# Kernel optimization log

Hardware: AMD Instinct MI355X
Metric: run time of the kernel (lower is better)

The kernel has to match this reference:

```python
import jax, jax.numpy as jnp
import numpy as np

B, D, NQ, NK, K = 8, 384, 2048, 2048, 8
NEG_SLOPE = 0.2


def setup_inputs() -> dict:
    key = jax.random.key(0)
    ks = jax.random.split(key, 6)
    return {
        "query_coords": jax.random.normal(ks[0], (B, 3, NQ), jnp.float32),
        "query_features": jax.random.normal(ks[1], (B, D, NQ), jnp.float32),
        "key_coords": jax.random.normal(ks[2], (B, 3, NK), jnp.float32),
        "key_features": jax.random.normal(ks[3], (B, D, NK), jnp.float32),
        "W": jax.random.normal(ks[4], (D, 2 * D), jnp.float32) / np.sqrt(2.0 * D),
        "b": jnp.zeros((D,), jnp.float32),
    }


def _knn_idx(qc, kc, k):
    # qc: [B,3,Nq], kc: [B,3,Nk] -> indices of k nearest keys per query [B,Nq,k]
    q2 = jnp.sum(qc * qc, axis=1)                      # [B,Nq]
    k2 = jnp.sum(kc * kc, axis=1)                      # [B,Nk]
    inner = jnp.einsum('bcq,bck->bqk', qc, kc)         # [B,Nq,Nk]
    dist = q2[:, :, None] - 2.0 * inner + k2[:, None, :]
    _, idx = jax.lax.top_k(-dist, k)
    return idx


def reference(query_coords, query_features, key_coords, key_features, W, b):
    idx = _knn_idx(query_coords, key_coords, K)        # [B,Nq,K]
    kf = jnp.transpose(key_features, (0, 2, 1))        # [B,Nk,D]
    qf = jnp.transpose(query_features, (0, 2, 1))      # [B,Nq,D]
    nbr = jax.vmap(lambda f, i: f[i])(kf, idx)         # gather -> [B,Nq,K,D]
    center = qf[:, :, None, :]                          # [B,Nq,1,D]
    # DGCNN/PoinTr graph feature: concat(neighbor - center, center)
    geom = jnp.concatenate(
        [nbr - center, jnp.broadcast_to(center, nbr.shape)], axis=-1)  # [B,Nq,K,2D]
    h = jnp.einsum('bqkf,df->bqkd', geom, W) + b        # Linear(2D -> D)
    h = jnp.where(h >= 0, h, NEG_SLOPE * h)             # LeakyReLU(0.2)
    return jnp.max(h, axis=2)                           # max over k -> [B,Nq,D]
```

## Files before the change

kernel.cpp:

```cpp
#include <hip/hip_runtime.h>
#include <hip/hip_bf16.h>
#include <float.h>

#define BB 8
#define DD 384
#define NQ 2048
#define NK 2048
#define NEG 0.2f

#define QPW 4

__global__ __launch_bounds__(256) void knn_kernel(
    const float* __restrict__ qc,
    const float* __restrict__ kc,
    int* __restrict__ idx)
{
  __shared__ float4 ksm[NK];

  const int b = blockIdx.y;
  const int t = threadIdx.x;

  const float* kcb = kc + (size_t)b * 3 * NK;
  for (int i = t; i < NK; i += 256) {
    float x = kcb[i], y = kcb[NK + i], z = kcb[2 * NK + i];
    ksm[i] = make_float4(x, y, z, (x * x + y * y) + z * z);
  }
  __syncthreads();

  const int w = t >> 6;
  const int l = t & 63;
  const float* qcb = qc + (size_t)b * 3 * NQ;

  for (int qi = 0; qi < QPW; ++qi) {
    const int q = blockIdx.x * (4 * QPW) + w * QPW + qi;
    const float qx = qcb[q], qy = qcb[NQ + q], qz = qcb[2 * NQ + q];
    const float q2 = (qx * qx + qy * qy) + qz * qz;

    float d[32];
    #pragma unroll
    for (int j = 0; j < 32; ++j) {
      float4 kv = ksm[j * 64 + l];
      float inner = (qx * kv.x + qy * kv.y) + qz * kv.z;
      d[j] = (q2 - 2.0f * inner) + kv.w;
    }

    int outk[8];
    #pragma unroll
    for (int r = 0; r < 8; ++r) {
      float m = d[0]; int mj = 0;
      #pragma unroll
      for (int j = 1; j < 32; ++j) {
        bool c = d[j] < m;
        m  = c ? d[j] : m;
        mj = c ? j : mj;
      }
      int mkey = mj * 64 + l;
      #pragma unroll
      for (int off = 32; off >= 1; off >>= 1) {
        float om = __shfl_xor(m, off);
        int   ok = __shfl_xor(mkey, off);
        bool take = (om < m) || (om == m && ok < mkey);
        m    = take ? om : m;
        mkey = take ? ok : mkey;
      }
      outk[r] = mkey;
      const bool mine = (l == (mkey & 63));
      const int  slot = mkey >> 6;
      #pragma unroll
      for (int j = 0; j < 32; ++j) {
        bool kill = mine && (j == slot);
        d[j] = kill ? FLT_MAX : d[j];
      }
    }

    int myv = outk[0];
    #pragma unroll
    for (int r = 1; r < 8; ++r) myv = (l == r) ? outk[r] : myv;
    if (l < 8) idx[((size_t)b * NQ + q) * 8 + l] = myv;
  }
}

__global__ __launch_bounds__(256) void proj_gemm_all(
    const float* __restrict__ kf,
    const float* __restrict__ qf,
    const float* __restrict__ W,
    const float* __restrict__ bias,
    float* __restrict__ pk,
    float* __restrict__ pq)
{
  __shared__ float At[16][128];
  __shared__ float Bt[16][132];

  const int t    = threadIdx.x;
  const int z    = blockIdx.z;
  const int b    = z & 7;
  const int mode = z >> 3;
  const int n0 = blockIdx.x * 128;
  const int d0 = blockIdx.y * 128;
  const int td = t & 15;
  const int tn = t >> 4;

  float acc[8][8];
  #pragma unroll
  for (int i = 0; i < 8; ++i)
    #pragma unroll
    for (int j = 0; j < 8; ++j) acc[i][j] = 0.f;

  const float* feats = mode ? qf : kf;
  float* out = mode ? pq : pk;
  const float* fb = feats + (size_t)b * DD * 2048;

  const int ar  = t >> 5;
  const int ac  = (t & 31) * 4;
  const int bdl = t >> 2;
  const int bf  = (t & 3) * 4;

  float4 sa0, sa1, sw1a, sw1b, sw2a, sw2b;

#define PREFETCH(KT)                                                           \
  {                                                                            \
    sa0 = *(const float4*)&fb[(size_t)((KT) + ar) * 2048 + n0 + ac];           \
    sa1 = *(const float4*)&fb[(size_t)((KT) + ar + 8) * 2048 + n0 + ac];       \
    const float* wr0 = W + (size_t)(d0 + bdl) * (2 * DD) + (KT) + bf;          \
    const float* wr1 = W + (size_t)(d0 + bdl + 64) * (2 * DD) + (KT) + bf;     \
    sw1a = *(const float4*)wr0;                                                \
    sw1b = *(const float4*)wr1;                                                \
    if (mode) { sw2a = *(const float4*)(wr0 + DD); sw2b = *(const float4*)(wr1 + DD); } \
  }

  PREFETCH(0);

  for (int kt = 0; kt < DD; kt += 16) {
    *(float4*)&At[ar][ac]     = sa0;
    *(float4*)&At[ar + 8][ac] = sa1;
    {
      float4 w = sw1a;
      if (mode) { w.x = sw2a.x - w.x; w.y = sw2a.y - w.y; w.z = sw2a.z - w.z; w.w = sw2a.w - w.w; }
      Bt[bf + 0][bdl] = w.x; Bt[bf + 1][bdl] = w.y;
      Bt[bf + 2][bdl] = w.z; Bt[bf + 3][bdl] = w.w;
    }
    {
      float4 w = sw1b;
      if (mode) { w.x = sw2b.x - w.x; w.y = sw2b.y - w.y; w.z = sw2b.z - w.z; w.w = sw2b.w - w.w; }
      Bt[bf + 0][bdl + 64] = w.x; Bt[bf + 1][bdl + 64] = w.y;
      Bt[bf + 2][bdl + 64] = w.z; Bt[bf + 3][bdl + 64] = w.w;
    }
    __syncthreads();

    if (kt + 16 < DD) PREFETCH(kt + 16);

    #pragma unroll
    for (int k = 0; k < 16; ++k) {
      float a[8], bb[8];
      {
        float4 v = *(const float4*)&At[k][tn * 4];
        a[0] = v.x; a[1] = v.y; a[2] = v.z; a[3] = v.w;
        v = *(const float4*)&At[k][tn * 4 + 64];
        a[4] = v.x; a[5] = v.y; a[6] = v.z; a[7] = v.w;
        v = *(const float4*)&Bt[k][td * 4];
        bb[0] = v.x; bb[1] = v.y; bb[2] = v.z; bb[3] = v.w;
        v = *(const float4*)&Bt[k][td * 4 + 64];
        bb[4] = v.x; bb[5] = v.y; bb[6] = v.z; bb[7] = v.w;
      }
      #pragma unroll
      for (int i = 0; i < 8; ++i)
        #pragma unroll
        for (int j = 0; j < 8; ++j)
          acc[i][j] = fmaf(a[i], bb[j], acc[i][j]);
    }
    __syncthreads();
  }
#undef PREFETCH

  float4 blo = make_float4(0.f, 0.f, 0.f, 0.f);
  float4 bhi = make_float4(0.f, 0.f, 0.f, 0.f);
  if (mode) {
    blo = *(const float4*)&bias[d0 + td * 4];
    bhi = *(const float4*)&bias[d0 + td * 4 + 64];
  }

  float* ob = out + (size_t)b * 2048 * DD;
  #pragma unroll
  for (int i = 0; i < 8; ++i) {
    int n = n0 + tn * 4 + (i & 3) + ((i >= 4) ? 64 : 0);
    float4 c0, c1;
    c0.x = acc[i][0] + blo.x; c0.y = acc[i][1] + blo.y;
    c0.z = acc[i][2] + blo.z; c0.w = acc[i][3] + blo.w;
    c1.x = acc[i][4] + bhi.x; c1.y = acc[i][5] + bhi.y;
    c1.z = acc[i][6] + bhi.z; c1.w = acc[i][7] + bhi.w;
    *(float4*)&ob[(size_t)n * DD + d0 + td * 4]      = c0;
    *(float4*)&ob[(size_t)n * DD + d0 + td * 4 + 64] = c1;
  }
}

__global__ __launch_bounds__(384) void gather_max_kernel(
    const float4* __restrict__ pk4,
    const float4* __restrict__ pq4,
    const int* __restrict__ idx,
    float4* __restrict__ out4)
{
  const int t   = threadIdx.x;
  const int bq0 = blockIdx.x * 4;
  __shared__ int nb[4][8];
  if (t < 32) nb[t >> 3][t & 7] = idx[(size_t)(bq0 + (t >> 3)) * 8 + (t & 7)];
  __syncthreads();

  const int q_l = t / 96;
  const int dv  = t - q_l * 96;
  const int bq  = bq0 + q_l;
  const int b   = bq >> 11;
  const float4* pkb = pk4 + (size_t)b * NK * 96;

  float4 m = make_float4(-FLT_MAX, -FLT_MAX, -FLT_MAX, -FLT_MAX);
  #pragma unroll
  for (int s = 0; s < 8; ++s) {
    float4 v = pkb[(size_t)nb[q_l][s] * 96 + dv];
    m.x = fmaxf(m.x, v.x); m.y = fmaxf(m.y, v.y);
    m.z = fmaxf(m.z, v.z); m.w = fmaxf(m.w, v.w);
  }
  float4 c = pq4[(size_t)bq * 96 + dv];
  float4 r;
  r.x = m.x + c.x; r.y = m.y + c.y; r.z = m.z + c.z; r.w = m.w + c.w;
  r.x = (r.x >= 0.f) ? r.x : NEG * r.x;
  r.y = (r.y >= 0.f) ? r.y : NEG * r.y;
  r.z = (r.z >= 0.f) ? r.z : NEG * r.z;
  r.w = (r.w >= 0.f) ? r.w : NEG * r.w;
  out4[(size_t)bq * 96 + dv] = r;
}

extern "C" void kernel_launch(void* const* d_in, const int* in_sizes, int n_in,
                              void* d_out, int out_size, void* d_ws, size_t ws_size,
                              hipStream_t stream) {
  const float* qc   = (const float*)d_in[0];
  const float* qf   = (const float*)d_in[1];
  const float* kc   = (const float*)d_in[2];
  const float* kf   = (const float*)d_in[3];
  const float* W    = (const float*)d_in[4];
  const float* bias = (const float*)d_in[5];
  float* out = (float*)d_out;

  char* ws = (char*)d_ws;
  float* pk = (float*)ws;
  float* pq = (float*)(ws + (size_t)BB * NK * DD * 4);
  int*   ix = (int*)  (ws + (size_t)2 * BB * NK * DD * 4);

  knn_kernel<<<dim3(NQ / (4 * QPW), BB), 256, 0, stream>>>(qc, kc, ix);
  proj_gemm_all<<<dim3(2048 / 128, DD / 128, 2 * BB), 256, 0, stream>>>(kf, qf, W, bias, pk, pq);
  gather_max_kernel<<<dim3(BB * NQ / 4), 384, 0, stream>>>(
      (const float4*)pk, (const float4*)pq, ix, (float4*)out);
}
```

Before: 304.2 us.

## Run projection GEMM on bf16 MFMA with split hi/lo operands

Adds pre-pass kernels that transpose the features and split them, along with the packed weights, into bf16 high and low halves. The projection GEMM then runs on MFMA 16x16x32 bf16 instructions using three products (hh, hl, lh) to approximate fp32 accuracy. pq is written straight into the output buffer so that less workspace is needed. This trades the FP32 FMA GEMM for matrix-core throughput, at the cost of extra packing passes, roughly 25MB of extra traffic and slightly lower precision. The old path is kept as a fallback when the workspace is too small.

```diff
diff --git a/kernel.cpp b/kernel.cpp
--- a/kernel.cpp
+++ b/kernel.cpp
@@ -8,18 +8,26 @@
 #define NK 2048
 #define NEG 0.2f
 
+typedef __attribute__((ext_vector_type(8))) __bf16 bf16x8v;
+typedef __attribute__((ext_vector_type(4))) float  float4v;
+
+__device__ __forceinline__ unsigned short bf16_rne(float x) {
+  unsigned int u = __float_as_uint(x);
+  return (unsigned short)((u + 0x7FFFu + ((u >> 16) & 1u)) >> 16);
+}
+__device__ __forceinline__ float bf16_to_f32(unsigned short h) {
+  return __uint_as_float(((unsigned int)h) << 16);
+}
+
 #define QPW 4
 
 __global__ __launch_bounds__(256) void knn_kernel(
-    const float* __restrict__ qc,
-    const float* __restrict__ kc,
+    const float* __restrict__ qc, const float* __restrict__ kc,
     int* __restrict__ idx)
 {
   __shared__ float4 ksm[NK];
-
   const int b = blockIdx.y;
   const int t = threadIdx.x;
-
   const float* kcb = kc + (size_t)b * 3 * NK;
   for (int i = t; i < NK; i += 256) {
     float x = kcb[i], y = kcb[NK + i], z = kcb[2 * NK + i];
@@ -27,8 +35,7 @@
   }
   __syncthreads();
 
-  const int w = t >> 6;
-  const int l = t & 63;
+  const int w = t >> 6, l = t & 63;
   const float* qcb = qc + (size_t)b * 3 * NQ;
 
   for (int qi = 0; qi < QPW; ++qi) {
@@ -72,7 +79,6 @@
         d[j] = kill ? FLT_MAX : d[j];
       }
     }
-
     int myv = outk[0];
     #pragma unroll
     for (int r = 1; r < 8; ++r) myv = (l == r) ? outk[r] : myv;
@@ -80,75 +86,204 @@
   }
 }
 
+__global__ __launch_bounds__(256) void transpose_pack_kernel(
+    const float* __restrict__ kf, const float* __restrict__ qf,
+    unsigned short* __restrict__ Apk)
+{
+  __shared__ float tile[64][68];
+  const int t = threadIdx.x;
+  const int z = blockIdx.z;
+  const int b = z & 7;
+  const float* src = ((z >> 3) ? qf : kf) + (size_t)b * DD * 2048;
+  const int f0 = blockIdx.y * 64;
+  const int n0 = blockIdx.x * 64;
+
+  {
+    const int fr = t >> 2, nc = (t & 3) * 16;
+    const float* p = src + (size_t)(f0 + fr) * 2048 + n0 + nc;
+    float4 v0 = *(const float4*)(p);
+    float4 v1 = *(const float4*)(p + 4);
+    float4 v2 = *(const float4*)(p + 8);
+    float4 v3 = *(const float4*)(p + 12);
+    *(float4*)&tile[fr][nc]      = v0;
+    *(float4*)&tile[fr][nc + 4]  = v1;
+    *(float4*)&tile[fr][nc + 8]  = v2;
+    *(float4*)&tile[fr][nc + 12] = v3;
+  }
+  __syncthreads();
+  {
+    const int nr = t >> 2, fc = (t & 3) * 16;
+    unsigned int hp[8], lp[8];
+    #pragma unroll
+    for (int i = 0; i < 8; ++i) {
+      float va = tile[fc + 2 * i][nr];
+      float vb = tile[fc + 2 * i + 1][nr];
+      unsigned short ha = bf16_rne(va), hb = bf16_rne(vb);
+      unsigned short la = bf16_rne(va - bf16_to_f32(ha));
+      unsigned short lb = bf16_rne(vb - bf16_to_f32(hb));
+      hp[i] = (unsigned int)ha | ((unsigned int)hb << 16);
+      lp[i] = (unsigned int)la | ((unsigned int)lb << 16);
+    }
+    unsigned short* row = Apk + ((size_t)z * 2048 + n0 + nr) * (2 * DD);
+    *(uint4*)(row + f0 + fc)          = make_uint4(hp[0], hp[1], hp[2], hp[3]);
+    *(uint4*)(row + f0 + fc + 8)      = make_uint4(hp[4], hp[5], hp[6], hp[7]);
+    *(uint4*)(row + DD + f0 + fc)     = make_uint4(lp[0], lp[1], lp[2], lp[3]);
+    *(uint4*)(row + DD + f0 + fc + 8) = make_uint4(lp[4], lp[5], lp[6], lp[7]);
+  }
+}
+
+__global__ __launch_bounds__(192) void wpack_kernel(
+    const float* __restrict__ W, unsigned short* __restrict__ Wpk)
+{
+  const int d = blockIdx.x;
+  const int mode = blockIdx.y;
+  const int t = threadIdx.x;
+  const float* wrow = W + (size_t)d * (2 * DD) + t * 2;
+  float2 w1 = *(const float2*)(wrow);
+  float a = w1.x, c = w1.y;
+  if (mode) {
+    float2 w2 = *(const float2*)(wrow + DD);
+    a = w2.x - a; c = w2.y - c;
+  }
+  unsigned short ha = bf16_rne(a), hc = bf16_rne(c);
+  unsigned short la = bf16_rne(a - bf16_to_f32(ha));
+  unsigned short lc = bf16_rne(c - bf16_to_f32(hc));
+  unsigned short* orow = Wpk + ((size_t)mode * DD + d) * (2 * DD);
+  *(unsigned int*)(orow + t * 2)      = (unsigned int)ha | ((unsigned int)hc << 16);
+  *(unsigned int*)(orow + DD + t * 2) = (unsigned int)la | ((unsigned int)lc << 16);
+}
+
+__global__ __launch_bounds__(256) void proj_gemm_mfma(
+    const unsigned short* __restrict__ Apk,
+    const unsigned short* __restrict__ Wpk,
+    const float* __restrict__ bias,
+    float* __restrict__ pk, float* __restrict__ pq)
+{
+  __shared__ unsigned short Alds[128][72];
+  __shared__ unsigned short Blds[128][72];
+
+  const int t = threadIdx.x;
+  const int z = blockIdx.z, b = z & 7, mode = z >> 3;
+  const int n0 = blockIdx.x * 128;
+  const int d0 = blockIdx.y * 128;
+  const int w = t >> 6, l = t & 63;
+  const int wn = w & 1, wd = w >> 1;
+  const int lr = l & 15, g = l >> 4;
+
+  float4v acc[4][4];
+  #pragma unroll
+  for (int i = 0; i < 4; ++i)
+    #pragma unroll
+    for (int j = 0; j < 4; ++j) acc[i][j] = (float4v){0.f, 0.f, 0.f, 0.f};
+
+  const int sr = t >> 1, sh = (t & 1) * 32;
+  const unsigned short* asrc = Apk + ((size_t)z * 2048 + n0 + sr) * (2 * DD) + (t & 1) * DD;
+  const unsigned short* bsrc = Wpk + ((size_t)mode * DD + d0 + sr) * (2 * DD) + (t & 1) * DD;
+
+  for (int ks = 0; ks < 12; ++ks) {
+    const int kt = ks * 32;
+    float4 a0 = *(const float4*)(asrc + kt);
+    float4 a1 = *(const float4*)(asrc + kt + 8);
+    float4 a2 = *(const float4*)(asrc + kt + 16);
+    float4 a3 = *(const float4*)(asrc + kt + 24);
+    float4 b0 = *(const float4*)(bsrc + kt);
+    float4 b1 = *(const float4*)(bsrc + kt + 8);
+    float4 b2 = *(const float4*)(bsrc + kt + 16);
+    float4 b3 = *(const float4*)(bsrc + kt + 24);
+    __syncthreads();
+    *(float4*)&Alds[sr][sh]      = a0;
+    *(float4*)&Alds[sr][sh + 8]  = a1;
+    *(float4*)&Alds[sr][sh + 16] = a2;
+    *(float4*)&Alds[sr][sh + 24] = a3;
+    *(float4*)&Blds[sr][sh]      = b0;
+    *(float4*)&Blds[sr][sh + 8]  = b1;
+    *(float4*)&Blds[sr][sh + 16] = b2;
+    *(float4*)&Blds[sr][sh + 24] = b3;
+    __syncthreads();
+
+    bf16x8v ah[4], al[4], bh[4], bl[4];
+    #pragma unroll
+    for (int i = 0; i < 4; ++i) {
+      ah[i] = *(const bf16x8v*)&Alds[wn * 64 + i * 16 + lr][g * 8];
+      al[i] = *(const bf16x8v*)&Alds[wn * 64 + i * 16 + lr][32 + g * 8];
+      bh[i] = *(const bf16x8v*)&Blds[wd * 64 + i * 16 + lr][g * 8];
+      bl[i] = *(const bf16x8v*)&Blds[wd * 64 + i * 16 + lr][32 + g * 8];
+    }
+    #pragma unroll
+    for (int i = 0; i < 4; ++i)
+      #pragma unroll
+      for (int j = 0; j < 4; ++j) {
+        acc[i][j] = __builtin_amdgcn_mfma_f32_16x16x32_bf16(ah[i], bh[j], acc[i][j], 0, 0, 0);
+        acc[i][j] = __builtin_amdgcn_mfma_f32_16x16x32_bf16(ah[i], bl[j], acc[i][j], 0, 0, 0);
+        acc[i][j] = __builtin_amdgcn_mfma_f32_16x16x32_bf16(al[i], bh[j], acc[i][j], 0, 0, 0);
+      }
+  }
+
+  float bv[4];
+  #pragma unroll
+  for (int j = 0; j < 4; ++j)
+    bv[j] = mode ? bias[d0 + wd * 64 + j * 16 + lr] : 0.f;
+
+  float* out = (mode ? pq : pk) + (size_t)b * 2048 * DD;
+  #pragma unroll
+  for (int i = 0; i < 4; ++i) {
+    const int nb_ = n0 + wn * 64 + i * 16 + g * 4;
+    #pragma unroll
+    for (int j = 0; j < 4; ++j) {
+      const int dcol = d0 + wd * 64 + j * 16 + lr;
+      #pragma unroll
+      for (int r = 0; r < 4; ++r)
+        out[(size_t)(nb_ + r) * DD + dcol] = acc[i][j][r] + bv[j];
+    }
+  }
+}
+
 __global__ __launch_bounds__(256) void proj_gemm_all(
-    const float* __restrict__ kf,
-    const float* __restrict__ qf,
-    const float* __restrict__ W,
-    const float* __restrict__ bias,
-    float* __restrict__ pk,
-    float* __restrict__ pq)
+    const float* __restrict__ kf, const float* __restrict__ qf,
+    const float* __restrict__ W, const float* __restrict__ bias,
+    float* __restrict__ pk, float* __restrict__ pq)
 {
   __shared__ float At[16][128];
   __shared__ float Bt[16][132];
-
-  const int t    = threadIdx.x;
-  const int z    = blockIdx.z;
-  const int b    = z & 7;
-  const int mode = z >> 3;
-  const int n0 = blockIdx.x * 128;
-  const int d0 = blockIdx.y * 128;
-  const int td = t & 15;
-  const int tn = t >> 4;
-
+  const int t = threadIdx.x;
+  const int z = blockIdx.z, b = z & 7, mode = z >> 3;
+  const int n0 = blockIdx.x * 128, d0 = blockIdx.y * 128;
+  const int td = t & 15, tn = t >> 4;
   float acc[8][8];
   #pragma unroll
   for (int i = 0; i < 8; ++i)
     #pragma unroll
     for (int j = 0; j < 8; ++j) acc[i][j] = 0.f;
-
   const float* feats = mode ? qf : kf;
   float* out = mode ? pq : pk;
   const float* fb = feats + (size_t)b * DD * 2048;
-
-  const int ar  = t >> 5;
-  const int ac  = (t & 31) * 4;
-  const int bdl = t >> 2;
-  const int bf  = (t & 3) * 4;
-
+  const int ar = t >> 5, ac = (t & 31) * 4, bdl = t >> 2, bf = (t & 3) * 4;
   float4 sa0, sa1, sw1a, sw1b, sw2a, sw2b;
-
 #define PREFETCH(KT)                                                           \
   {                                                                            \
     sa0 = *(const float4*)&fb[(size_t)((KT) + ar) * 2048 + n0 + ac];           \
     sa1 = *(const float4*)&fb[(size_t)((KT) + ar + 8) * 2048 + n0 + ac];       \
     const float* wr0 = W + (size_t)(d0 + bdl) * (2 * DD) + (KT) + bf;          \
     const float* wr1 = W + (size_t)(d0 + bdl + 64) * (2 * DD) + (KT) + bf;     \
-    sw1a = *(const float4*)wr0;                                                \
-    sw1b = *(const float4*)wr1;                                                \
+    sw1a = *(const float4*)wr0; sw1b = *(const float4*)wr1;                    \
     if (mode) { sw2a = *(const float4*)(wr0 + DD); sw2b = *(const float4*)(wr1 + DD); } \
   }
-
   PREFETCH(0);
-
   for (int kt = 0; kt < DD; kt += 16) {
     *(float4*)&At[ar][ac]     = sa0;
     *(float4*)&At[ar + 8][ac] = sa1;
     {
       float4 w = sw1a;
       if (mode) { w.x = sw2a.x - w.x; w.y = sw2a.y - w.y; w.z = sw2a.z - w.z; w.w = sw2a.w - w.w; }
-      Bt[bf + 0][bdl] = w.x; Bt[bf + 1][bdl] = w.y;
-      Bt[bf + 2][bdl] = w.z; Bt[bf + 3][bdl] = w.w;
+      Bt[bf + 0][bdl] = w.x; Bt[bf + 1][bdl] = w.y; Bt[bf + 2][bdl] = w.z; Bt[bf + 3][bdl] = w.w;
     }
     {
       float4 w = sw1b;
       if (mode) { w.x = sw2b.x - w.x; w.y = sw2b.y - w.y; w.z = sw2b.z - w.z; w.w = sw2b.w - w.w; }
-      Bt[bf + 0][bdl + 64] = w.x; Bt[bf + 1][bdl + 64] = w.y;
-      Bt[bf + 2][bdl + 64] = w.z; Bt[bf + 3][bdl + 64] = w.w;
+      Bt[bf + 0][bdl + 64] = w.x; Bt[bf + 1][bdl + 64] = w.y; Bt[bf + 2][bdl + 64] = w.z; Bt[bf + 3][bdl + 64] = w.w;
     }
     __syncthreads();
-
     if (kt + 16 < DD) PREFETCH(kt + 16);
-
     #pragma unroll
     for (int k = 0; k < 16; ++k) {
       float a[8], bb[8];
@@ -171,14 +306,12 @@
     __syncthreads();
   }
 #undef PREFETCH
-
   float4 blo = make_float4(0.f, 0.f, 0.f, 0.f);
   float4 bhi = make_float4(0.f, 0.f, 0.f, 0.f);
   if (mode) {
     blo = *(const float4*)&bias[d0 + td * 4];
     bhi = *(const float4*)&bias[d0 + td * 4 + 64];
   }
-
   float* ob = out + (size_t)b * 2048 * DD;
   #pragma unroll
   for (int i = 0; i < 8; ++i) {
@@ -194,23 +327,19 @@
 }
 
 __global__ __launch_bounds__(384) void gather_max_kernel(
-    const float4* __restrict__ pk4,
-    const float4* __restrict__ pq4,
-    const int* __restrict__ idx,
-    float4* __restrict__ out4)
-{
-  const int t   = threadIdx.x;
+    const float4* __restrict__ pk4, const float4* pq4,
+    const int* __restrict__ idx, float4* out4)
+{
+  const int t = threadIdx.x;
   const int bq0 = blockIdx.x * 4;
   __shared__ int nb[4][8];
   if (t < 32) nb[t >> 3][t & 7] = idx[(size_t)(bq0 + (t >> 3)) * 8 + (t & 7)];
   __syncthreads();
-
   const int q_l = t / 96;
   const int dv  = t - q_l * 96;
   const int bq  = bq0 + q_l;
   const int b   = bq >> 11;
   const float4* pkb = pk4 + (size_t)b * NK * 96;
-
   float4 m = make_float4(-FLT_MAX, -FLT_MAX, -FLT_MAX, -FLT_MAX);
   #pragma unroll
   for (int s = 0; s < 8; ++s) {
@@ -238,14 +367,33 @@
   const float* W    = (const float*)d_in[4];
   const float* bias = (const float*)d_in[5];
   float* out = (float*)d_out;
-
   char* ws = (char*)d_ws;
-  float* pk = (float*)ws;
-  float* pq = (float*)(ws + (size_t)BB * NK * DD * 4);
-  int*   ix = (int*)  (ws + (size_t)2 * BB * NK * DD * 4);
-
-  knn_kernel<<<dim3(NQ / (4 * QPW), BB), 256, 0, stream>>>(qc, kc, ix);
-  proj_gemm_all<<<dim3(2048 / 128, DD / 128, 2 * BB), 256, 0, stream>>>(kf, qf, W, bias, pk, pq);
-  gather_max_kernel<<<dim3(BB * NQ / 4), 384, 0, stream>>>(
-      (const float4*)pk, (const float4*)pq, ix, (float4*)out);
-}
+
+  const size_t APK_BYTES = (size_t)16 * 2048 * (2 * DD) * 2;
+  const size_t WPK_BYTES = (size_t)2 * DD * (2 * DD) * 2;
+  const size_t PK_BYTES  = (size_t)BB * NK * DD * 4;
+  const size_t IDX_BYTES = (size_t)BB * NQ * 8 * 4;
+
+  if (ws_size >= APK_BYTES + WPK_BYTES + PK_BYTES + IDX_BYTES) {
+    unsigned short* Apk = (unsigned short*)ws;
+    unsigned short* Wpk = (unsigned short*)(ws + APK_BYTES);
+    float* pk = (float*)(ws + APK_BYTES + WPK_BYTES);
+    int*   ix = (int*)  (ws + APK_BYTES + WPK_BYTES + PK_BYTES);
+    float* pq = out;
+
+    transpose_pack_kernel<<<dim3(32, 6, 16), 256, 0, stream>>>(kf, qf, Apk);
+    wpack_kernel<<<dim3(DD, 2), 192, 0, stream>>>(W, Wpk);
+    knn_kernel<<<dim3(NQ / (4 * QPW), BB), 256, 0, stream>>>(qc, kc, ix);
+    proj_gemm_mfma<<<dim3(16, 3, 16), 256, 0, stream>>>(Apk, Wpk, bias, pk, pq);
+    gather_max_kernel<<<dim3(BB * NQ / 4), 384, 0, stream>>>(
+        (const float4*)pk, (const float4*)pq, ix, (float4*)out);
+  } else {
+    float* pk = (float*)ws;
+    float* pq = (float*)(ws + PK_BYTES);
+    int*   ix = (int*)  (ws + 2 * PK_BYTES);
+    knn_kernel<<<dim3(NQ / (4 * QPW), BB), 256, 0, stream>>>(qc, kc, ix);
+    proj_gemm_all<<<dim3(16, 3, 16), 256, 0, stream>>>(kf, qf, W, bias, pk, pq);
+    gather_max_kernel<<<dim3(BB * NQ / 4), 384, 0, stream>>>(
+        (const float4*)pk, (const float4*)pq, ix, (float4*)out);
+  }
+}
```

Result: faster. 264.4 us (-13.1%).
